# Kernel tuning notes

Measured on AMD Instinct MI355X. Metric: run time of the kernel, lower is better.

Reference implementation:

```python
import jax, jax.numpy as jnp
import numpy as np

N = 524288          # total atoms (sorted by degree)
E = 1433600         # total directed bonds
B, L = 16384, 32    # molecules x atoms-per-molecule (B*L == N)
NODE, EDGE, H, OUT = 64, 16, 128, 128
N0 = 8192           # number of degree-0 atoms
DEG_COUNTS = {1: 65536, 2: 131072, 3: 196608, 4: 98304, 5: 24576}
BN_EPS = 1e-5


def setup_inputs() -> dict:
    key = jax.random.key(0)
    ks = jax.random.split(key, 24)
    inp = {}
    inp["node_feat"] = jax.random.normal(ks[0], (N, NODE), jnp.float32)
    inp["edge_feat"] = jax.random.normal(ks[1], (E, EDGE), jnp.float32)
    i = 2
    for d in (1, 2, 3, 4, 5):
        n_d = DEG_COUNTS[d]
        inp[f"nbr_node_d{d}"] = jax.random.randint(ks[i], (n_d, d), 0, N, jnp.int32); i += 1
        inp[f"nbr_edge_d{d}"] = jax.random.randint(ks[i], (n_d, d), 0, E, jnp.int32); i += 1
    inp["atom_index"] = jnp.arange(B * L, dtype=jnp.int32).reshape(B, L)

    def lin(k, o, fan_in):
        return jax.random.normal(k, (o, fan_in), jnp.float32) / np.sqrt(fan_in).astype(np.float32)

    inp["out_W0"] = lin(ks[12], OUT, NODE); inp["out_b0"] = jnp.zeros((OUT,), jnp.float32)
    inp["out_W1"] = lin(ks[13], OUT, H);    inp["out_b1"] = jnp.zeros((OUT,), jnp.float32)
    inp["out_W2"] = lin(ks[14], OUT, H);    inp["out_b2"] = jnp.zeros((OUT,), jnp.float32)
    inp["conv0_selfW"] = lin(ks[15], H, NODE)
    inp["conv0_degW"] = jax.random.normal(ks[16], (5, H, NODE + EDGE), jnp.float32) / np.sqrt(NODE + EDGE).astype(np.float32)
    inp["conv0_bias"] = jnp.zeros((1, H), jnp.float32)
    inp["conv1_selfW"] = lin(ks[17], H, H)
    inp["conv1_degW"] = jax.random.normal(ks[18], (5, H, H + EDGE), jnp.float32) / np.sqrt(H + EDGE).astype(np.float32)
    inp["conv1_bias"] = jnp.zeros((1, H), jnp.float32)
    return inp


def _graph_degree_conv(node_repr, edge_repr, selfW, degW, bias, nbr_nodes, nbr_edges):
    out_size = selfW.shape[0]
    # degree 0: zero neighbor contribution
    parts = [jnp.zeros((N0, out_size), node_repr.dtype)]
    for di, d in enumerate((1, 2, 3, 4, 5)):
        nn_rep = node_repr[nbr_nodes[di]]          # [n_d, d, node]
        ee_rep = edge_repr[nbr_edges[di]]          # [n_d, d, edge]
        summed = jnp.concatenate([nn_rep.sum(1), ee_rep.sum(1)], axis=-1)  # [n_d, node+edge]
        parts.append(summed @ degW[di].T)          # per-degree linear (no bias)
    neighbor_repr = jnp.concatenate(parts, axis=0)  # nodes sorted by degree -> aligned
    act = node_repr @ selfW.T + neighbor_repr + bias
    # BatchNorm1d(affine=False), training-mode batch stats (biased variance)
    mean = act.mean(0)
    var = act.var(0)
    act = (act - mean) / jnp.sqrt(var + BN_EPS)
    return jax.nn.relu(act)


def reference(node_feat, edge_feat,
              nbr_node_d1, nbr_edge_d1, nbr_node_d2, nbr_edge_d2,
              nbr_node_d3, nbr_edge_d3, nbr_node_d4, nbr_edge_d4,
              nbr_node_d5, nbr_edge_d5, atom_index,
              out_W0, out_b0, out_W1, out_b1, out_W2, out_b2,
              conv0_selfW, conv0_degW, conv0_bias,
              conv1_selfW, conv1_degW, conv1_bias):
    nbr_nodes = (nbr_node_d1, nbr_node_d2, nbr_node_d3, nbr_node_d4, nbr_node_d5)
    nbr_edges = (nbr_edge_d1, nbr_edge_d2, nbr_edge_d3, nbr_edge_d4, nbr_edge_d5)

    x = node_feat
    acc = jax.nn.softmax(x @ out_W0.T + out_b0, axis=1)
    x = _graph_degree_conv(x, edge_feat, conv0_selfW, conv0_degW, conv0_bias, nbr_nodes, nbr_edges)
    acc = acc + jax.nn.softmax(x @ out_W1.T + out_b1, axis=1)
    x = _graph_degree_conv(x, edge_feat, conv1_selfW, conv1_degW, conv1_bias, nbr_nodes, nbr_edges)
    acc = acc + jax.nn.softmax(x @ out_W2.T + out_b2, axis=1)
    # scatter per-atom activations into [batch, max_len, OUT]
    return acc[atom_index]
```

## Files before the change

kernel.cpp:

```cpp
#include <hip/hip_runtime.h>
#include <hip/hip_bf16.h>
#include <math.h>


typedef short  short8   __attribute__((ext_vector_type(8)));
typedef unsigned short ushort8v __attribute__((ext_vector_type(8)));
typedef float  f32x4    __attribute__((ext_vector_type(4)));
typedef unsigned int u32;

static constexpr int  N_ATOMS = 524288;
static constexpr long NROWCOL = (long)N_ATOMS * 128;
static constexpr int  NBLK    = N_ATOMS / 64;

__device__ __forceinline__ float bf2f(ushort h) {
    return __uint_as_float(((unsigned)h) << 16);
}
__device__ __forceinline__ ushort f2bf(float x) {
    unsigned u = __float_as_uint(x);
    return (ushort)((u + 0x7fffu + ((u >> 16) & 1u)) >> 16);
}

__device__ __forceinline__ uint4 pack8(const float v[8]) {
    union { __hip_bfloat162 h2[4]; uint4 u; } c;
#pragma unroll
    for (int e = 0; e < 4; ++e)
        c.h2[e] = __float22bfloat162_rn(make_float2(v[2*e], v[2*e+1]));
    return c.u;
}
__device__ __forceinline__ short8 pack8s(const float v[8]) {
    union { uint4 u; short8 s; } c;
    c.u = pack8(v);
    return c.s;
}
__device__ __forceinline__ ushort f2bf1(float x) {
    union { __hip_bfloat16 b; ushort u; } c;
    c.b = __float2bfloat16(x);
    return c.u;
}

__device__ __forceinline__ void gload_lds16(const ushort* g, ushort* l) {
    __builtin_amdgcn_global_load_lds(
        (const __attribute__((address_space(1))) u32*)g,
        (__attribute__((address_space(3))) u32*)l, 16, 0, 0);
}

__device__ __forceinline__ void seg_of(long r, int& d, long& off) {
    if      (r < 73728)  { d = 1; off = 8192;  }
    else if (r < 204800) { d = 2; off = 73728; }
    else if (r < 401408) { d = 3; off = 204800;}
    else if (r < 499712) { d = 4; off = 401408;}
    else                 { d = 5; off = 499712;}
}

__global__ __launch_bounds__(256)
void nodeb_kernel(const float* __restrict__ node, ushort* __restrict__ node_b)
{
    const long i = (long)blockIdx.x * 256 + threadIdx.x;
    const float4* p = (const float4*)(node + i * 8);
    const float4 a = p[0], b = p[1];
    const float v[8] = {a.x,a.y,a.z,a.w,b.x,b.y,b.z,b.w};
    *(uint4*)(node_b + i * 8) = pack8(v);
}

__global__ __launch_bounds__(256)
void esum_kernel(const float* __restrict__ edge_feat,
                 const int* __restrict__ ne1, const int* __restrict__ ne2,
                 const int* __restrict__ ne3, const int* __restrict__ ne4,
                 const int* __restrict__ ne5, ushort* __restrict__ esumb)
{
    const long t = (long)blockIdx.x * 256 + threadIdx.x;
    const long r = 8192 + (t >> 1);
    const int  h = (int)(t & 1);
    int d; long off; seg_of(r, d, off);
    const int* ne = (d==1)?ne1:(d==2)?ne2:(d==3)?ne3:(d==4)?ne4:ne5;
    const long i0 = (r - off) * d;
    float v[8] = {0,0,0,0,0,0,0,0};
    for (int j = 0; j < d; ++j) {
        const long e = ne[i0 + j];
        const float4* p = (const float4*)(edge_feat + e * 16 + h * 8);
        const float4 a = p[0], b = p[1];
        v[0]+=a.x; v[1]+=a.y; v[2]+=a.z; v[3]+=a.w;
        v[4]+=b.x; v[5]+=b.y; v[6]+=b.z; v[7]+=b.w;
    }
    *(uint4*)(esumb + (r - 8192) * 16 + h * 8) = pack8(v);
}

__global__ void wprep(const float* __restrict__ src, ushort* __restrict__ dst,
                      int rows, int Ks, int Kd)
{
    const int i = blockIdx.x * 256 + threadIdx.x;
    if (i >= rows * Kd) return;
    const int r = i / Kd, c = i % Kd;
    dst[i] = f2bf(c < Ks ? src[r * Ks + c] : 0.f);
}

__global__ void wprep_img(const float* __restrict__ src, ushort* __restrict__ dst, int K)
{
    const int i = blockIdx.x * 256 + threadIdx.x;
    if (i >= 128 * K) return;
    const int row = i / K, col = i % K;
    dst[(col >> 3) * 1024 + row * 8 + (col & 7)] = f2bf(src[i]);
}

template<int NG, bool BN>
__device__ __forceinline__ void stage_rows(const ushort* __restrict__ X, long r0,
                                           ushort* __restrict__ Ab,
                                           const float* __restrict__ statsL)
{
    for (int t = threadIdx.x; t < 64 * NG; t += 256) {
        const int row = t / NG, g = t % NG;
        const long gr = r0 + row;
        uint4 w;
        if (BN) {
            const int c0 = g * 8;
            const ushort8v u = *(const ushort8v*)(X + gr * (long)(NG * 8) + g * 8);
            float v[8];
#pragma unroll
            for (int e = 0; e < 8; ++e)
                v[e] = fmaxf(fmaf(bf2f(u[e]), statsL[c0 + e], statsL[128 + c0 + e]), 0.f);
            w = pack8(v);
        } else {
            w = *(const uint4*)(X + gr * (long)(NG * 8) + g * 8);
        }
        ((uint4*)Ab)[row * NG + (g ^ (row & 7))] = w;
    }
}

template<int NGL, int NST, int NGN, bool BN>
__device__ __forceinline__ void stage_gather(const ushort* __restrict__ X,
                                             const ushort* __restrict__ esumb,
                                             const int* __restrict__ nnl, int d,
                                             long r0, ushort* __restrict__ Ab,
                                             const float* __restrict__ statsL)
{
    constexpr int KINW = NGN * 8;
    for (int t = threadIdx.x; t < 64 * NST; t += 256) {
        const int row = t / NST, g = t % NST;
        uint4 w = {0, 0, 0, 0};
        if (g < NGN) {
            const int c0 = g * 8;
            float v[8] = {0,0,0,0,0,0,0,0};
            for (int j = 0; j < d; ++j) {
                const long idx = nnl[row * d + j];
                const ushort8v u = *(const ushort8v*)(X + idx * (long)KINW + c0);
#pragma unroll
                for (int e = 0; e < 8; ++e) {
                    float x = bf2f(u[e]);
                    if (BN) x = fmaxf(fmaf(x, statsL[c0 + e], statsL[128 + c0 + e]), 0.f);
                    v[e] += x;
                }
            }
            w = pack8(v);
        } else if (g < NGN + 2) {
            const long er = r0 + row - 8192;
            w = *(const uint4*)(esumb + er * 16 + (g - NGN) * 8);
        }
        ((uint4*)Ab)[row * NGL + (g ^ (row & 7))] = w;
    }
}

template<int KS, int NG>
__device__ __forceinline__ void mfma_lds(const ushort* __restrict__ Ab,
                                         const ushort* __restrict__ Wb, int KP,
                                         int wc, f32x4 acc[4][2])
{
    const int lane = threadIdx.x & 63;
    const int lg = lane >> 4, lr = lane & 15;
#pragma unroll
    for (int ks = 0; ks < KS; ++ks) {
        short8 B0 = *(const short8*)(Wb + (long)(wc + lr) * KP + ks * 32 + 8 * lg);
        short8 B1 = *(const short8*)(Wb + (long)(wc + 16 + lr) * KP + ks * 32 + 8 * lg);
        const int gk = ks * 4 + lg;
#pragma unroll
        for (int m = 0; m < 4; ++m) {
            const int row = 16 * m + lr;
            const short8 a = *(const short8*)(Ab + (row * NG + (gk ^ (row & 7))) * 8);
            acc[m][0] = __builtin_amdgcn_mfma_f32_16x16x32_bf16(a, B0, acc[m][0], 0, 0, 0);
            acc[m][1] = __builtin_amdgcn_mfma_f32_16x16x32_bf16(a, B1, acc[m][1], 0, 0, 0);
        }
    }
}

template<int K1, bool BNIN, bool NTST, int NGL2, int NST2, int NGN2, int KS2, int KP2>
__global__ __launch_bounds__(256, 2)
void conv_kernel(const ushort* __restrict__ X, const ushort* __restrict__ Wb1,
                 const ushort* __restrict__ Wb2base,
                 const int* __restrict__ nn1, const int* __restrict__ nn2,
                 const int* __restrict__ nn3, const int* __restrict__ nn4,
                 const int* __restrict__ nn5,
                 const ushort* __restrict__ esumb, const float* __restrict__ cbias,
                 const float* __restrict__ stats_in,
                 ushort* __restrict__ act_out, float* __restrict__ part)
{
    constexpr int NG1 = K1 / 8;
    constexpr int KS1 = K1 / 32;
    constexpr int NGMAX = (NGL2 > NG1) ? NGL2 : NG1;
    __shared__ uint4 AbV[64 * NGMAX];
    __shared__ int   nnl[320];
    __shared__ float statsL[256];
    ushort* Ab = (ushort*)AbV;

    const long r0 = (long)blockIdx.x * 64;
    const int wid = threadIdx.x >> 6, lane = threadIdx.x & 63;
    const int lg = lane >> 4, lr = lane & 15, wc = wid * 32;

    if (BNIN)
        for (int t = threadIdx.x; t < 256; t += 256) statsL[t] = stats_in[t];

    int d = 0;
    const bool has2 = (r0 >= 8192);
    if (has2) {
        long off; seg_of(r0, d, off);
        const int* nn = (d==1)?nn1:(d==2)?nn2:(d==3)?nn3:(d==4)?nn4:nn5;
        const long i0 = (r0 - off) * d;
        for (int t = threadIdx.x; t < 64 * d; t += 256) nnl[t] = nn[i0 + t];
    }
    __syncthreads();

    stage_rows<NG1, BNIN>(X, r0, Ab, statsL);
    __syncthreads();
    f32x4 acc[4][2] = {};
    mfma_lds<KS1, NG1>(Ab, Wb1, K1, wc, acc);

    if (has2) {
        __syncthreads();
        stage_gather<NGL2, NST2, NGN2, BNIN>(X, esumb, nnl, d, r0, Ab, statsL);
        __syncthreads();
        const ushort* Wb2 = Wb2base + (long)(d - 1) * 128 * KP2;
        mfma_lds<KS2, NGL2>(Ab, Wb2, KP2, wc, acc);
    }

#pragma unroll
    for (int n = 0; n < 2; ++n) {
        const float bv = cbias[wc + n * 16 + lr];
#pragma unroll
        for (int m = 0; m < 4; ++m)
#pragma unroll
            for (int j = 0; j < 4; ++j) acc[m][n][j] += bv;
    }
#pragma unroll
    for (int m = 0; m < 4; ++m)
#pragma unroll
        for (int j = 0; j < 4; ++j) {
            const long row = r0 + 16 * m + 4 * lg + j;
#pragma unroll
            for (int n = 0; n < 2; ++n) {
                ushort* p = &act_out[row * 128 + wc + n * 16 + lr];
                const ushort hv = f2bf1(acc[m][n][j]);
                if (NTST) __builtin_nontemporal_store(hv, p);
                else      *p = hv;
            }
        }
#pragma unroll
    for (int n = 0; n < 2; ++n) {
        float s = 0.f, q = 0.f;
#pragma unroll
        for (int m = 0; m < 4; ++m)
#pragma unroll
            for (int j = 0; j < 4; ++j) { const float v = acc[m][n][j]; s += v; q += v * v; }
        s += __shfl_xor(s, 16); s += __shfl_xor(s, 32);
        q += __shfl_xor(q, 16); q += __shfl_xor(q, 32);
        if (lane < 16) {
            __builtin_nontemporal_store(s, &part[(long)blockIdx.x * 256 + wc + n * 16 + lr]);
            __builtin_nontemporal_store(q, &part[(long)blockIdx.x * 256 + 128 + wc + n * 16 + lr]);
        }
    }
}

__global__ __launch_bounds__(256)
void bn_finalize(const float* __restrict__ part, float* __restrict__ stats)
{
    const int c = blockIdx.x;
    float s = 0.f, q = 0.f;
    for (int b = threadIdx.x; b < NBLK; b += 256) {
        s += part[(long)b * 256 + c];
        q += part[(long)b * 256 + 128 + c];
    }
#pragma unroll
    for (int o = 1; o < 64; o <<= 1) { s += __shfl_xor(s, o); q += __shfl_xor(q, o); }
    __shared__ float rs[4], rq[4];
    const int wid = threadIdx.x >> 6;
    if ((threadIdx.x & 63) == 0) { rs[wid] = s; rq[wid] = q; }
    __syncthreads();
    if (threadIdx.x == 0) {
        s = rs[0] + rs[1] + rs[2] + rs[3];
        q = rq[0] + rq[1] + rq[2] + rq[3];
        const float mean = s * (1.0f / N_ATOMS);
        const float var  = q * (1.0f / N_ATOMS) - mean * mean;
        const float rstd = 1.0f / sqrtf(var + 1e-5f);
        stats[c]       = rstd;
        stats[128 + c] = -mean * rstd;
    }
}

__device__ __forceinline__ void mfma8_img(const ushort* __restrict__ Wl,
                                          int ks, int lg, int lr,
                                          short8 af, f32x4 (&acc)[8])
{
    const int a0 = (ks * 4 + lg) * 1024 + lr * 8;
#pragma unroll
    for (int n = 0; n < 8; ++n) {
        const short8 bf = *(const short8*)(Wl + a0 + n * 128);
        acc[n] = __builtin_amdgcn_mfma_f32_16x16x32_bf16(af, bf, acc[n], 0, 0, 0);
    }
}

__device__ __forceinline__ short8 cvt_bn(short8 u, int k0, const float* __restrict__ sl)
{
    float v[8];
#pragma unroll
    for (int e = 0; e < 8; ++e)
        v[e] = fmaxf(fmaf(bf2f((ushort)u[e]), sl[k0 + e], sl[128 + k0 + e]), 0.f);
    return pack8s(v);
}

__device__ __forceinline__ void softmax_accum(f32x4 (&acc)[8],
                                              const float* __restrict__ bias,
                                              int lr, f32x4 (&oacc)[8])
{
    float bb[8];
#pragma unroll
    for (int n = 0; n < 8; ++n) bb[n] = bias[n * 16 + lr];
#pragma unroll
    for (int j = 0; j < 4; ++j) {
        float s = 0.f;
#pragma unroll
        for (int n = 0; n < 8; ++n) {
            const float e = __expf(acc[n][j] + bb[n]);
            acc[n][j] = e; s += e;
        }
        s += __shfl_xor(s, 1); s += __shfl_xor(s, 2);
        s += __shfl_xor(s, 4); s += __shfl_xor(s, 8);
        const float inv = 1.0f / s;
#pragma unroll
        for (int n = 0; n < 8; ++n) oacc[n][j] += acc[n][j] * inv;
    }
}

__global__ __launch_bounds__(256, 4)
void out_kernel(const ushort* __restrict__ node_b, const ushort* __restrict__ act0b,
                const ushort* __restrict__ act1b, const ushort* __restrict__ wimg,
                const float* __restrict__ b0, const float* __restrict__ b1,
                const float* __restrict__ b2,
                const float* __restrict__ stats0, const float* __restrict__ stats1,
                float* __restrict__ out)
{
    __shared__ ushort Wlds[16384];
    __shared__ float sl[512];

    const int wid = threadIdx.x >> 6, lane = threadIdx.x & 63;
    const int lg = lane >> 4, lr = lane & 15;
    const long rA = (long)blockIdx.x * 64 + wid * 16 + lr;

#pragma unroll
    for (int i = 0; i < 8; ++i) {
        const int c = wid * 8 + i;
        gload_lds16(wimg + 8192 + c * 512 + lane * 8, &Wlds[c * 512]);
    }
    for (int t = threadIdx.x; t < 512; t += 256)
        sl[t] = (t < 256) ? stats0[t] : stats1[t - 256];

    short8 r1[4];
#pragma unroll
    for (int ks = 0; ks < 4; ++ks)
        r1[ks] = *(const short8*)(act0b + rA * 128 + ks * 32 + lg * 8);
    short8 r0a = *(const short8*)(node_b + rA * 64 + lg * 8);

    __syncthreads();

    f32x4 oacc[8] = {};
    f32x4 acc[8] = {};
    {
#pragma unroll
        for (int ks = 0; ks < 4; ++ks)
            mfma8_img(Wlds, ks, lg, lr, cvt_bn(r1[ks], ks * 32 + lg * 8, sl), acc);
    }
    short8 r0b = *(const short8*)(node_b + rA * 64 + 32 + lg * 8);
    short8 r2[4];
#pragma unroll
    for (int ks = 0; ks < 4; ++ks)
        r2[ks] = *(const short8*)(act1b + rA * 128 + ks * 32 + lg * 8);

    softmax_accum(acc, b1, lr, oacc);

    __syncthreads();
#pragma unroll
    for (int i = 0; i < 4; ++i) {
        const int c = wid * 4 + i;
        gload_lds16(wimg + c * 512 + lane * 8, &Wlds[c * 512]);
    }
    __syncthreads();

#pragma unroll
    for (int n = 0; n < 8; ++n) acc[n] = f32x4{0.f, 0.f, 0.f, 0.f};
    {
        mfma8_img(Wlds, 0, lg, lr, r0a, acc);
        mfma8_img(Wlds, 1, lg, lr, r0b, acc);
    }
    softmax_accum(acc, b0, lr, oacc);

    __syncthreads();
#pragma unroll
    for (int i = 0; i < 8; ++i) {
        const int c = wid * 8 + i;
        gload_lds16(wimg + 24576 + c * 512 + lane * 8, &Wlds[c * 512]);
    }
    __syncthreads();

#pragma unroll
    for (int n = 0; n < 8; ++n) acc[n] = f32x4{0.f, 0.f, 0.f, 0.f};
    {
#pragma unroll
        for (int ks = 0; ks < 4; ++ks)
            mfma8_img(Wlds, ks, lg, lr, cvt_bn(r2[ks], ks * 32 + lg * 8, sl + 256), acc);
    }
    softmax_accum(acc, b2, lr, oacc);

    const long rC0 = (long)blockIdx.x * 64 + wid * 16;
#pragma unroll
    for (int j = 0; j < 4; ++j) {
        const long row = rC0 + 4 * lg + j;
#pragma unroll
        for (int n = 0; n < 8; ++n)
            __builtin_nontemporal_store(oacc[n][j], &out[row * 128 + n * 16 + lr]);
    }
}

extern "C" void kernel_launch(void* const* d_in, const int* in_sizes, int n_in,
                              void* d_out, int out_size, void* d_ws, size_t ws_size,
                              hipStream_t stream)
{
    const float* node_feat = (const float*)d_in[0];
    const float* edge_feat = (const float*)d_in[1];
    const int* nn1 = (const int*)d_in[2];  const int* ne1 = (const int*)d_in[3];
    const int* nn2 = (const int*)d_in[4];  const int* ne2 = (const int*)d_in[5];
    const int* nn3 = (const int*)d_in[6];  const int* ne3 = (const int*)d_in[7];
    const int* nn4 = (const int*)d_in[8];  const int* ne4 = (const int*)d_in[9];
    const int* nn5 = (const int*)d_in[10]; const int* ne5 = (const int*)d_in[11];
    const float* W0     = (const float*)d_in[13];
    const float* b0     = (const float*)d_in[14];
    const float* W1     = (const float*)d_in[15];
    const float* b1     = (const float*)d_in[16];
    const float* W2     = (const float*)d_in[17];
    const float* b2     = (const float*)d_in[18];
    const float* selfW0 = (const float*)d_in[19];
    const float* degW0  = (const float*)d_in[20];
    const float* cb0    = (const float*)d_in[21];
    const float* selfW1 = (const float*)d_in[22];
    const float* degW1  = (const float*)d_in[23];
    const float* cb1    = (const float*)d_in[24];

    float*  part   = (float*)d_ws;
    float*  stats0 = part + (long)NBLK * 256;
    float*  stats1 = stats0 + 256;
    ushort* act0b  = (ushort*)(stats1 + 256);
    ushort* act1b  = act0b + NROWCOL;
    ushort* node_b = act1b + NROWCOL;
    ushort* esumb  = node_b + (long)N_ATOMS * 64;
    ushort* wb_self0 = esumb + (long)516096 * 16;
    ushort* wb_deg0  = wb_self0 + 128 * 64;
    ushort* wb_self1 = wb_deg0  + 640 * 96;
    ushort* wb_deg1  = wb_self1 + 128 * 128;
    ushort* wimg     = wb_deg1  + 640 * 160;
    const size_t needed = (size_t)((char*)(wimg + 40960) - (char*)d_ws);
    if (ws_size < needed) return;

    wprep<<<(128*64 +255)/256, 256, 0, stream>>>(selfW0, wb_self0, 128, 64, 64);
    wprep<<<(640*96 +255)/256, 256, 0, stream>>>(degW0,  wb_deg0,  640, 80, 96);
    wprep<<<(128*128+255)/256, 256, 0, stream>>>(selfW1, wb_self1, 128, 128, 128);
    wprep<<<(640*160+255)/256, 256, 0, stream>>>(degW1,  wb_deg1,  640, 144, 160);
    wprep_img<<<(128*64 +255)/256, 256, 0, stream>>>(W0, wimg,          64);
    wprep_img<<<(128*128+255)/256, 256, 0, stream>>>(W1, wimg + 8192,  128);
    wprep_img<<<(128*128+255)/256, 256, 0, stream>>>(W2, wimg + 24576, 128);
    nodeb_kernel<<<(int)((long)N_ATOMS * 64 / 8 / 256), 256, 0, stream>>>(node_feat, node_b);

    esum_kernel<<<4032, 256, 0, stream>>>(edge_feat, ne1, ne2, ne3, ne4, ne5, esumb);

    conv_kernel<64, false, false, 16, 12, 8, 3, 96><<<NBLK, 256, 0, stream>>>(
        node_b, wb_self0, wb_deg0, nn1, nn2, nn3, nn4, nn5, esumb, cb0,
        nullptr, act0b, part);
    bn_finalize<<<128, 256, 0, stream>>>(part, stats0);

    conv_kernel<128, true, true, 24, 20, 16, 5, 160><<<NBLK, 256, 0, stream>>>(
        act0b, wb_self1, wb_deg1, nn1, nn2, nn3, nn4, nn5, esumb, cb1,
        stats0, act1b, part);
    bn_finalize<<<128, 256, 0, stream>>>(part, stats1);

    out_kernel<<<NBLK, 256, 0, stream>>>(node_b, act0b, act1b, wimg,
        b0, b1, b2, stats0, stats1, (float*)d_out);
}
```

Measured before the change: 518.8 us.

## Split conv kernel output columns across eight waves instead of four

The conv kernel now launches 512 threads per block, and each of the eight waves computes one 16-column slice of the 128 output channels instead of two slices. The staging loops stride by 512, so more threads share the gather and staging work and more latency can be hidden. In exchange each wave reuses each A fragment read from LDS for only one MFMA, which doubles LDS A-reads per block. The launch bounds ask for 8 blocks per CU, which may force the register allocation down.

```diff
diff --git a/kernel.cpp b/kernel.cpp
--- a/kernel.cpp
+++ b/kernel.cpp
@@ -107,7 +107,7 @@
                                            ushort* __restrict__ Ab,
                                            const float* __restrict__ statsL)
 {
-    for (int t = threadIdx.x; t < 64 * NG; t += 256) {
+    for (int t = threadIdx.x; t < 64 * NG; t += 512) {
         const int row = t / NG, g = t % NG;
         const long gr = r0 + row;
         uint4 w;
@@ -134,7 +134,7 @@
                                              const float* __restrict__ statsL)
 {
     constexpr int KINW = NGN * 8;
-    for (int t = threadIdx.x; t < 64 * NST; t += 256) {
+    for (int t = threadIdx.x; t < 64 * NST; t += 512) {
         const int row = t / NST, g = t % NST;
         uint4 w = {0, 0, 0, 0};
         if (g < NGN) {
@@ -162,27 +162,25 @@
 template<int KS, int NG>
 __device__ __forceinline__ void mfma_lds(const ushort* __restrict__ Ab,
                                          const ushort* __restrict__ Wb, int KP,
-                                         int wc, f32x4 acc[4][2])
+                                         int wc, f32x4 acc[4])
 {
     const int lane = threadIdx.x & 63;
     const int lg = lane >> 4, lr = lane & 15;
 #pragma unroll
     for (int ks = 0; ks < KS; ++ks) {
         short8 B0 = *(const short8*)(Wb + (long)(wc + lr) * KP + ks * 32 + 8 * lg);
-        short8 B1 = *(const short8*)(Wb + (long)(wc + 16 + lr) * KP + ks * 32 + 8 * lg);
         const int gk = ks * 4 + lg;
 #pragma unroll
         for (int m = 0; m < 4; ++m) {
             const int row = 16 * m + lr;
             const short8 a = *(const short8*)(Ab + (row * NG + (gk ^ (row & 7))) * 8);
-            acc[m][0] = __builtin_amdgcn_mfma_f32_16x16x32_bf16(a, B0, acc[m][0], 0, 0, 0);
-            acc[m][1] = __builtin_amdgcn_mfma_f32_16x16x32_bf16(a, B1, acc[m][1], 0, 0, 0);
+            acc[m] = __builtin_amdgcn_mfma_f32_16x16x32_bf16(a, B0, acc[m], 0, 0, 0);
         }
     }
 }
 
 template<int K1, bool BNIN, bool NTST, int NGL2, int NST2, int NGN2, int KS2, int KP2>
-__global__ __launch_bounds__(256, 2)
+__global__ __launch_bounds__(512, 8)
 void conv_kernel(const ushort* __restrict__ X, const ushort* __restrict__ Wb1,
                  const ushort* __restrict__ Wb2base,
                  const int* __restrict__ nn1, const int* __restrict__ nn2,
@@ -202,10 +200,10 @@
 
     const long r0 = (long)blockIdx.x * 64;
     const int wid = threadIdx.x >> 6, lane = threadIdx.x & 63;
-    const int lg = lane >> 4, lr = lane & 15, wc = wid * 32;
+    const int lg = lane >> 4, lr = lane & 15, wc = wid * 16;
 
     if (BNIN)
-        for (int t = threadIdx.x; t < 256; t += 256) statsL[t] = stats_in[t];
+        for (int t = threadIdx.x; t < 256; t += 512) statsL[t] = stats_in[t];
 
     int d = 0;
     const bool has2 = (r0 >= 8192);
@@ -213,13 +211,13 @@
         long off; seg_of(r0, d, off);
         const int* nn = (d==1)?nn1:(d==2)?nn2:(d==3)?nn3:(d==4)?nn4:nn5;
         const long i0 = (r0 - off) * d;
-        for (int t = threadIdx.x; t < 64 * d; t += 256) nnl[t] = nn[i0 + t];
+        for (int t = threadIdx.x; t < 64 * d; t += 512) nnl[t] = nn[i0 + t];
     }
     __syncthreads();
 
     stage_rows<NG1, BNIN>(X, r0, Ab, statsL);
     __syncthreads();
-    f32x4 acc[4][2] = {};
+    f32x4 acc[4] = {};
     mfma_lds<KS1, NG1>(Ab, Wb1, K1, wc, acc);
 
     if (has2) {
@@ -230,39 +228,34 @@
         mfma_lds<KS2, NGL2>(Ab, Wb2, KP2, wc, acc);
     }
 
-#pragma unroll
-    for (int n = 0; n < 2; ++n) {
-        const float bv = cbias[wc + n * 16 + lr];
-#pragma unroll
-        for (int m = 0; m < 4; ++m)
-#pragma unroll
-            for (int j = 0; j < 4; ++j) acc[m][n][j] += bv;
-    }
+    const float bv = cbias[wc + lr];
+#pragma unroll
+    for (int m = 0; m < 4; ++m)
+#pragma unroll
+        for (int j = 0; j < 4; ++j) acc[m][j] += bv;
+
 #pragma unroll
     for (int m = 0; m < 4; ++m)
 #pragma unroll
         for (int j = 0; j < 4; ++j) {
             const long row = r0 + 16 * m + 4 * lg + j;
-#pragma unroll
-            for (int n = 0; n < 2; ++n) {
-                ushort* p = &act_out[row * 128 + wc + n * 16 + lr];
-                const ushort hv = f2bf1(acc[m][n][j]);
-                if (NTST) __builtin_nontemporal_store(hv, p);
-                else      *p = hv;
-            }
-        }
-#pragma unroll
-    for (int n = 0; n < 2; ++n) {
+            ushort* p = &act_out[row * 128 + wc + lr];
+            const ushort hv = f2bf1(acc[m][j]);
+            if (NTST) __builtin_nontemporal_store(hv, p);
+            else      *p = hv;
+        }
+
+    {
         float s = 0.f, q = 0.f;
 #pragma unroll
         for (int m = 0; m < 4; ++m)
 #pragma unroll
-            for (int j = 0; j < 4; ++j) { const float v = acc[m][n][j]; s += v; q += v * v; }
+            for (int j = 0; j < 4; ++j) { const float v = acc[m][j]; s += v; q += v * v; }
         s += __shfl_xor(s, 16); s += __shfl_xor(s, 32);
         q += __shfl_xor(q, 16); q += __shfl_xor(q, 32);
         if (lane < 16) {
-            __builtin_nontemporal_store(s, &part[(long)blockIdx.x * 256 + wc + n * 16 + lr]);
-            __builtin_nontemporal_store(q, &part[(long)blockIdx.x * 256 + 128 + wc + n * 16 + lr]);
+            __builtin_nontemporal_store(s, &part[(long)blockIdx.x * 256 + wc + lr]);
+            __builtin_nontemporal_store(q, &part[(long)blockIdx.x * 256 + 128 + wc + lr]);
         }
     }
 }
@@ -476,12 +469,12 @@
 
     esum_kernel<<<4032, 256, 0, stream>>>(edge_feat, ne1, ne2, ne3, ne4, ne5, esumb);
 
-    conv_kernel<64, false, false, 16, 12, 8, 3, 96><<<NBLK, 256, 0, stream>>>(
+    conv_kernel<64, false, false, 16, 12, 8, 3, 96><<<NBLK, 512, 0, stream>>>(
         node_b, wb_self0, wb_deg0, nn1, nn2, nn3, nn4, nn5, esumb, cb0,
         nullptr, act0b, part);
     bn_finalize<<<128, 256, 0, stream>>>(part, stats0);
 
-    conv_kernel<128, true, true, 24, 20, 16, 5, 160><<<NBLK, 256, 0, stream>>>(
+    conv_kernel<128, true, true, 24, 20, 16, 5, 160><<<NBLK, 512, 0, stream>>>(
         act0b, wb_self1, wb_deg1, nn1, nn2, nn3, nn4, nn5, esumb, cb1,
         stats0, act1b, part);
     bn_finalize<<<128, 256, 0, stream>>>(part, stats1);
```

Result: slower. 538.6 us (+3.8%).
